# Kernel optimization log

Hardware: AMD Instinct MI355X
Metric: run time of the kernel (lower is better)

## Reference

```python
import jax, jax.numpy as jnp
import numpy as np

IGNORE_INDEX = 255


def setup_inputs() -> dict:
    key = jax.random.key(0)
    k1, k2 = jax.random.split(key)
    n, h, w = 8, 256, 256
    num_class, cnum = 20, 4
    c = num_class * cnum
    P = 8192  # number of parcel segments
    features = jax.random.normal(k1, (n, c, h, w), dtype=jnp.float32)
    parcel = jax.random.randint(k2, (n, h, w), 0, P, dtype=jnp.int32)
    # all pixels of a parcel share one class label (as the torch code assumes)
    target = (parcel % num_class).astype(jnp.int32)
    return {"features": features, "target": target, "parcel": parcel,
            "num_segments": P, "cnum": cnum, "num_class": num_class}


def reference(features, target, parcel, num_segments, cnum, num_class):
    n, c, h, w = features.shape
    hw = h * w
    # n c h w -> n (h w) c
    fea = features.reshape(n, c, hw).transpose(0, 2, 1)
    # MaxPool1d(cnum, stride=cnum) over channel dim: group consecutive cnum channels
    branch_dis = fea.reshape(n, hw, num_class, cnum).max(axis=-1)  # [n, hw, num_class]
    branch_dis = branch_dis.reshape(n * hw, num_class)

    t = target.reshape(-1)
    p = parcel.reshape(-1)
    valid = t != IGNORE_INDEX
    wgt = valid.astype(branch_dis.dtype)

    # fused segment-mean replacing the python loop over unique parcel ids
    seg_sum = jax.ops.segment_sum(branch_dis * wgt[:, None], p, num_segments=num_segments)
    counts = jax.ops.segment_sum(wgt, p, num_segments=num_segments)
    seg_mean = seg_sum / jnp.maximum(counts, 1.0)[:, None]  # [P, num_class]

    # per-parcel target (labels are constant within a parcel -> max == first)
    t_masked = jnp.where(valid, t, -1)
    tgt_parcel = jax.ops.segment_max(t_masked, p, num_segments=num_segments)
    seg_valid = (counts > 0).astype(seg_mean.dtype)

    logp = jax.nn.log_softmax(seg_mean, axis=-1)
    tgt_safe = jnp.clip(tgt_parcel, 0, num_class - 1)
    nll = -jnp.take_along_axis(logp, tgt_safe[:, None], axis=1)[:, 0]
    loss_dis = jnp.sum(nll * seg_valid) / jnp.maximum(jnp.sum(seg_valid), 1.0)

    # diversity branch: softmax over spatial dim, channel-group maxpool
    branch_div = jax.nn.softmax(fea, axis=1)  # softmax over hw
    branch_div = branch_div.reshape(n, hw, num_class, cnum).max(axis=-1)
    loss_div = 1.0 - jnp.mean(jnp.sum(branch_div, axis=1)) / num_class
    return loss_dis, loss_div
```

## Files before the change

### kernel.cpp

```cpp
#include <hip/hip_runtime.h>
#include <float.h>

#define IGNORE_INDEX 255

constexpr int N_IMG = 8;
constexpr int C     = 80;
constexpr int HW    = 65536;
constexpr int NC    = 20;
constexpr int CNUM  = 4;
constexpr int P     = 8192;
constexpr int NPIX  = N_IMG * HW;
constexpr int STRIPES = 4;
constexpr int NCH   = N_IMG * C;

constexpr size_t B_BDS   = 0;
constexpr size_t B_CNT   = (size_t)NPIX * 20 * 4;
constexpr size_t B_ACC   = B_CNT + (size_t)P * 4;
constexpr size_t B_OFF   = B_ACC + 64;
constexpr size_t B_WOFF  = B_OFF + (size_t)P * 4;
constexpr size_t B_PM    = B_WOFF + (size_t)P * 4;
constexpr size_t B_PS    = B_PM + (size_t)NCH * STRIPES * 4;
constexpr size_t B_CHOFF = B_PS + (size_t)NCH * STRIPES * 4;
constexpr size_t B_TGT   = B_CHOFF + (size_t)NCH * 4;
constexpr size_t NEED    = B_TGT + (size_t)P * 4;

__device__ __forceinline__ float waveMax(float v) {
#pragma unroll
  for (int o = 32; o > 0; o >>= 1) v = fmaxf(v, __shfl_down(v, o, 64));
  return v;
}
__device__ __forceinline__ float waveSum(float v) {
#pragma unroll
  for (int o = 32; o > 0; o >>= 1) v += __shfl_down(v, o, 64);
  return v;
}

__global__ __launch_bounds__(256) void stats_hist_kernel(
    const float* __restrict__ f, const int* __restrict__ target,
    const int* __restrict__ parcel, float* __restrict__ pm,
    float* __restrict__ ps, int* __restrict__ cnt) {
  if (blockIdx.x >= NCH * STRIPES) {
    const int t4 = (blockIdx.x - NCH * STRIPES) * 256 + threadIdx.x;
    const int4 tv = ((const int4*)target)[t4];
    const int4 pv = ((const int4*)parcel)[t4];
    if (tv.x != IGNORE_INDEX) atomicAdd(&cnt[pv.x], 1);
    if (tv.y != IGNORE_INDEX) atomicAdd(&cnt[pv.y], 1);
    if (tv.z != IGNORE_INDEX) atomicAdd(&cnt[pv.z], 1);
    if (tv.w != IGNORE_INDEX) atomicAdd(&cnt[pv.w], 1);
    return;
  }
  const int ch = blockIdx.x >> 2, stripe = blockIdx.x & 3;
  const float4* base =
      (const float4*)(f + (size_t)ch * HW + (size_t)stripe * (HW / STRIPES));
  const int n4 = HW / STRIPES / 4;
  float m = -FLT_MAX;
  for (int i = threadIdx.x; i < n4; i += 256) {
    float4 v = base[i];
    m = fmaxf(m, fmaxf(fmaxf(v.x, v.y), fmaxf(v.z, v.w)));
  }
  __shared__ float sred[4];
  __shared__ float bcast;
  const int wid = threadIdx.x >> 6, lid = threadIdx.x & 63;
  float wm = waveMax(m);
  if (lid == 0) sred[wid] = wm;
  __syncthreads();
  if (threadIdx.x == 0)
    bcast = fmaxf(fmaxf(sred[0], sred[1]), fmaxf(sred[2], sred[3]));
  __syncthreads();
  const float M = bcast;
  float s = 0.f;
  for (int i = threadIdx.x; i < n4; i += 256) {
    float4 v = base[i];
    s += __expf(v.x - M) + __expf(v.y - M) + __expf(v.z - M) + __expf(v.w - M);
  }
  float wsv = waveSum(s);
  __syncthreads();
  if (lid == 0) sred[wid] = wsv;
  __syncthreads();
  if (threadIdx.x == 0) {
    pm[blockIdx.x] = M;
    ps[blockIdx.x] = sred[0] + sred[1] + sred[2] + sred[3];
  }
}

__global__ __launch_bounds__(1024) void combine_scan_kernel(
    const float* __restrict__ pm, const float* __restrict__ ps,
    float* __restrict__ choff, const int* __restrict__ cnt,
    int* __restrict__ offs, int* __restrict__ woff) {
  const int t = threadIdx.x;
  if (t < NCH) {
    float m = -FLT_MAX;
#pragma unroll
    for (int i = 0; i < STRIPES; i++) m = fmaxf(m, pm[t * STRIPES + i]);
    float s = 0.f;
#pragma unroll
    for (int i = 0; i < STRIPES; i++)
      s += ps[t * STRIPES + i] * __expf(pm[t * STRIPES + i] - m);
    choff[t] = m + logf(s);
  }
  __shared__ int sh[1024];
  const int4* c4 = (const int4*)(cnt + t * 8);
  int4 a = c4[0], b = c4[1];
  int c[8] = {a.x, a.y, a.z, a.w, b.x, b.y, b.z, b.w};
  int tot = 0;
#pragma unroll
  for (int j = 0; j < 8; j++) tot += c[j];
  sh[t] = tot;
  __syncthreads();
  for (int d = 1; d < 1024; d <<= 1) {
    int v = (t >= d) ? sh[t - d] : 0;
    __syncthreads();
    sh[t] += v;
    __syncthreads();
  }
  int e = sh[t] - tot;
#pragma unroll
  for (int j = 0; j < 8; j++) {
    offs[t * 8 + j] = e;
    woff[t * 8 + j] = e;
    e += c[j];
  }
}

__global__ __launch_bounds__(256) void divbd_scatter_kernel(
    const float* __restrict__ f, const int* __restrict__ target,
    const int* __restrict__ parcel, const float* __restrict__ choff,
    int* __restrict__ woff, float* __restrict__ bds, int* __restrict__ tgtp,
    float* __restrict__ div_acc) {
  const int pg = blockIdx.x * 256 + threadIdx.x;
  const int img = pg >> 16;
  const int pix = pg & (HW - 1);
  const float* fb = f + (size_t)img * C * HW + pix;
  __shared__ float soff[C];
  if (threadIdx.x < C) soff[threadIdx.x] = choff[img * C + threadIdx.x];
  __syncthreads();
  float dm[NC];
  float divs = 0.f;
#pragma unroll
  for (int k = 0; k < NC; k++) {
    float d = -FLT_MAX, e = -FLT_MAX;
#pragma unroll
    for (int j = 0; j < CNUM; j++) {
      const int ch = k * CNUM + j;
      float v = fb[(size_t)ch * HW];
      d = fmaxf(d, v);
      e = fmaxf(e, v - soff[ch]);
    }
    dm[k] = d;
    divs += __expf(e);
  }
  const int t = target[pg];
  const int p = parcel[pg];
  if (t != IGNORE_INDEX) {
    const int pos = atomicAdd(&woff[p], 1);
    float4* o = (float4*)(bds + (size_t)pos * NC);
    o[0] = make_float4(dm[0], dm[1], dm[2], dm[3]);
    o[1] = make_float4(dm[4], dm[5], dm[6], dm[7]);
    o[2] = make_float4(dm[8], dm[9], dm[10], dm[11]);
    o[3] = make_float4(dm[12], dm[13], dm[14], dm[15]);
    o[4] = make_float4(dm[16], dm[17], dm[18], dm[19]);
    tgtp[p] = t;
  }
  __shared__ float sred[4];
  const int wid = threadIdx.x >> 6, lid = threadIdx.x & 63;
  float wsum = waveSum(divs);
  if (lid == 0) sred[wid] = wsum;
  __syncthreads();
  if (threadIdx.x == 0)
    atomicAdd(div_acc, sred[0] + sred[1] + sred[2] + sred[3]);
}

__global__ __launch_bounds__(256) void parcel_kernel(
    const float* __restrict__ bds, const int* __restrict__ cnt,
    const int* __restrict__ offs, const int* __restrict__ tgtp,
    float* __restrict__ acc) {
  const int wid = threadIdx.x >> 6, lid = threadIdx.x & 63;
  const int p = blockIdx.x * 4 + wid;
  const int c = cnt[p];
  float sums[NC];
#pragma unroll
  for (int k = 0; k < NC; k++) sums[k] = 0.f;
  if (c > 0) {
    const int start = offs[p];
    for (int i = lid; i < c; i += 64) {
      const float4* b = (const float4*)(bds + (size_t)(start + i) * NC);
      float4 b0 = b[0], b1 = b[1], b2 = b[2], b3 = b[3], b4 = b[4];
      sums[0] += b0.x;  sums[1] += b0.y;  sums[2] += b0.z;  sums[3] += b0.w;
      sums[4] += b1.x;  sums[5] += b1.y;  sums[6] += b1.z;  sums[7] += b1.w;
      sums[8] += b2.x;  sums[9] += b2.y;  sums[10] += b2.z; sums[11] += b2.w;
      sums[12] += b3.x; sums[13] += b3.y; sums[14] += b3.z; sums[15] += b3.w;
      sums[16] += b4.x; sums[17] += b4.y; sums[18] += b4.z; sums[19] += b4.w;
    }
  }
#pragma unroll
  for (int o = 32; o > 0; o >>= 1) {
#pragma unroll
    for (int k = 0; k < NC; k++) sums[k] += __shfl_xor(sums[k], o, 64);
  }
  float nll = 0.f, val = 0.f;
  if (c > 0) {
    const float inv = 1.f / (float)c;
    float mean[NC];
    float m = -FLT_MAX;
#pragma unroll
    for (int k = 0; k < NC; k++) {
      mean[k] = sums[k] * inv;
      m = fmaxf(m, mean[k]);
    }
    float se = 0.f;
#pragma unroll
    for (int k = 0; k < NC; k++) se += __expf(mean[k] - m);
    const float lse = m + logf(se);
    const int t = min(max(tgtp[p], 0), NC - 1);
    nll = lse - mean[t];
    val = 1.f;
  }
  __shared__ float sn[4], sv[4];
  if (lid == 0) { sn[wid] = nll; sv[wid] = val; }
  __syncthreads();
  if (threadIdx.x == 0) {
    atomicAdd(&acc[1], sn[0] + sn[1] + sn[2] + sn[3]);
    atomicAdd(&acc[2], sv[0] + sv[1] + sv[2] + sv[3]);
  }
}

__global__ void finalize_kernel(const float* __restrict__ acc,
                                float* __restrict__ out) {
  out[0] = acc[1] / fmaxf(acc[2], 1.f);
  out[1] = 1.f - acc[0] / (float)(N_IMG * NC * NC);
}

constexpr size_t OFF_SEGSUM = 0;
constexpr size_t OFF_COUNTS = 163840;
constexpr size_t OFF_CHOFF  = 172032;
constexpr size_t OFF_ACC    = 172672;
constexpr size_t BYTE_TGT   = 690752;
constexpr size_t BYTE_ZERO  = 690752;
constexpr size_t BYTE_TGT_N = P * sizeof(int);

__global__ __launch_bounds__(256) void chan_stats_fb(
    const float* __restrict__ f, float* __restrict__ chan_off) {
  const int ch = blockIdx.x;
  const float4* base = (const float4*)(f + (size_t)ch * HW);
  const int n4 = HW / 4;
  float m = -FLT_MAX;
  for (int i = threadIdx.x; i < n4; i += 256) {
    float4 v = base[i];
    m = fmaxf(m, fmaxf(fmaxf(v.x, v.y), fmaxf(v.z, v.w)));
  }
  __shared__ float sred[4];
  __shared__ float bcast;
  const int wid = threadIdx.x >> 6, lid = threadIdx.x & 63;
  float wm = waveMax(m);
  if (lid == 0) sred[wid] = wm;
  __syncthreads();
  if (threadIdx.x == 0)
    bcast = fmaxf(fmaxf(sred[0], sred[1]), fmaxf(sred[2], sred[3]));
  __syncthreads();
  const float M = bcast;
  float s = 0.f;
  for (int i = threadIdx.x; i < n4; i += 256) {
    float4 v = base[i];
    s += __expf(v.x - M) + __expf(v.y - M) + __expf(v.z - M) + __expf(v.w - M);
  }
  float wsv = waveSum(s);
  __syncthreads();
  if (lid == 0) sred[wid] = wsv;
  __syncthreads();
  if (threadIdx.x == 0)
    chan_off[ch] = M + logf(sred[0] + sred[1] + sred[2] + sred[3]);
}

__global__ __launch_bounds__(256) void pixel_fb(
    const float* __restrict__ f, const int* __restrict__ target,
    const int* __restrict__ parcel, const float* __restrict__ chan_off,
    float* __restrict__ seg_sum, float* __restrict__ counts,
    int* __restrict__ tgtp, float* __restrict__ div_acc) {
  const int t4 = blockIdx.x * 256 + threadIdx.x;
  const int img = t4 / (HW / 4);
  const int pix0 = (t4 % (HW / 4)) * 4;
  const float* fb = f + (size_t)img * C * HW;
  __shared__ float soff[C];
  if (threadIdx.x < C) soff[threadIdx.x] = chan_off[img * C + threadIdx.x];
  __syncthreads();
  const int4 tv = *(const int4*)(target + (size_t)img * HW + pix0);
  const int4 pv = *(const int4*)(parcel + (size_t)img * HW + pix0);
  int tarr[4] = {tv.x, tv.y, tv.z, tv.w};
  int parr[4] = {pv.x, pv.y, pv.z, pv.w};
  bool val[4];
#pragma unroll
  for (int i = 0; i < 4; i++) val[i] = (tarr[i] != IGNORE_INDEX);
  float divs = 0.f;
#pragma unroll
  for (int k = 0; k < NC; k++) {
    float4 dmax = make_float4(-FLT_MAX, -FLT_MAX, -FLT_MAX, -FLT_MAX);
    float4 em = make_float4(-FLT_MAX, -FLT_MAX, -FLT_MAX, -FLT_MAX);
#pragma unroll
    for (int j = 0; j < CNUM; j++) {
      const int ch = k * CNUM + j;
      float4 v = *(const float4*)(fb + (size_t)ch * HW + pix0);
      const float off = soff[ch];
      dmax.x = fmaxf(dmax.x, v.x); dmax.y = fmaxf(dmax.y, v.y);
      dmax.z = fmaxf(dmax.z, v.z); dmax.w = fmaxf(dmax.w, v.w);
      em.x = fmaxf(em.x, v.x - off); em.y = fmaxf(em.y, v.y - off);
      em.z = fmaxf(em.z, v.z - off); em.w = fmaxf(em.w, v.w - off);
    }
    divs += __expf(em.x) + __expf(em.y) + __expf(em.z) + __expf(em.w);
    float dmv[4] = {dmax.x, dmax.y, dmax.z, dmax.w};
#pragma unroll
    for (int i = 0; i < 4; i++)
      if (val[i]) atomicAdd(&seg_sum[parr[i] * NC + k], dmv[i]);
  }
#pragma unroll
  for (int i = 0; i < 4; i++) {
    if (val[i]) {
      atomicAdd(&counts[parr[i]], 1.0f);
      atomicMax(&tgtp[parr[i]], tarr[i]);
    }
  }
  __shared__ float sred[4];
  const int wid = threadIdx.x >> 6, lid = threadIdx.x & 63;
  float wsum = waveSum(divs);
  if (lid == 0) sred[wid] = wsum;
  __syncthreads();
  if (threadIdx.x == 0)
    atomicAdd(div_acc, sred[0] + sred[1] + sred[2] + sred[3]);
}

__global__ __launch_bounds__(256) void seg_fb(
    const float* __restrict__ seg_sum, const float* __restrict__ counts,
    const int* __restrict__ tgtp, float* __restrict__ nll_acc,
    float* __restrict__ vcnt_acc) {
  const int s = blockIdx.x * 256 + threadIdx.x;
  const float cntv = counts[s];
  const float valid = (cntv > 0.f) ? 1.f : 0.f;
  const float inv = 1.f / fmaxf(cntv, 1.f);
  float mean[NC];
  float m = -FLT_MAX;
#pragma unroll
  for (int k = 0; k < NC; k++) {
    mean[k] = seg_sum[s * NC + k] * inv;
    m = fmaxf(m, mean[k]);
  }
  float se = 0.f;
#pragma unroll
  for (int k = 0; k < NC; k++) se += __expf(mean[k] - m);
  const float lse = m + logf(se);
  int t = tgtp[s];
  t = min(max(t, 0), NC - 1);
  const float nll = (lse - mean[t]) * valid;
  __shared__ float sn[4], sv[4];
  const int wid = threadIdx.x >> 6, lid = threadIdx.x & 63;
  float wn = waveSum(nll);
  float wv = waveSum(valid);
  if (lid == 0) { sn[wid] = wn; sv[wid] = wv; }
  __syncthreads();
  if (threadIdx.x == 0) {
    atomicAdd(nll_acc, sn[0] + sn[1] + sn[2] + sn[3]);
    atomicAdd(vcnt_acc, sv[0] + sv[1] + sv[2] + sv[3]);
  }
}

extern "C" void kernel_launch(void* const* d_in, const int* in_sizes, int n_in,
                              void* d_out, int out_size, void* d_ws,
                              size_t ws_size, hipStream_t stream) {
  const float* features = (const float*)d_in[0];
  const int*   target   = (const int*)d_in[1];
  const int*   parcel   = (const int*)d_in[2];
  float* out = (float*)d_out;
  char* wsb = (char*)d_ws;

  if (ws_size >= NEED) {
    float* bds   = (float*)(wsb + B_BDS);
    int*   cnt   = (int*)(wsb + B_CNT);
    float* acc   = (float*)(wsb + B_ACC);
    int*   offs  = (int*)(wsb + B_OFF);
    int*   woff  = (int*)(wsb + B_WOFF);
    float* pm    = (float*)(wsb + B_PM);
    float* ps    = (float*)(wsb + B_PS);
    float* choff = (float*)(wsb + B_CHOFF);
    int*   tgtp  = (int*)(wsb + B_TGT);

    hipMemsetAsync(wsb + B_CNT, 0, P * 4 + 64, stream);

    stats_hist_kernel<<<NCH * STRIPES + NPIX / 1024, 256, 0, stream>>>(
        features, target, parcel, pm, ps, cnt);
    combine_scan_kernel<<<1, 1024, 0, stream>>>(pm, ps, choff, cnt, offs,
                                                woff);
    divbd_scatter_kernel<<<NPIX / 256, 256, 0, stream>>>(
        features, target, parcel, choff, woff, bds, tgtp, acc + 0);
    parcel_kernel<<<P / 4, 256, 0, stream>>>(bds, cnt, offs, tgtp, acc);
    finalize_kernel<<<1, 1, 0, stream>>>(acc, out);
  } else {
    float* ws       = (float*)d_ws;
    float* seg_sum  = ws + OFF_SEGSUM;
    float* counts   = ws + OFF_COUNTS;
    float* chan_off = ws + OFF_CHOFF;
    float* acc      = ws + OFF_ACC;
    int*   tgtp     = (int*)(wsb + BYTE_TGT);

    hipMemsetAsync(d_ws, 0, BYTE_ZERO, stream);
    hipMemsetAsync(wsb + BYTE_TGT, 0xFF, BYTE_TGT_N, stream);
    chan_stats_fb<<<NCH, 256, 0, stream>>>(features, chan_off);
    pixel_fb<<<NPIX / 4 / 256, 256, 0, stream>>>(features, target, parcel,
                                                 chan_off, seg_sum, counts,
                                                 tgtp, acc + 0);
    seg_fb<<<P / 256, 256, 0, stream>>>(seg_sum, counts, tgtp, acc + 1,
                                        acc + 2);
    finalize_kernel<<<1, 1, 0, stream>>>(acc, out);
  }
}
```

Before: 381.6 us.

## Write maxpool results densely by pixel and scatter only indices per parcel

```diff
diff --git a/kernel.cpp b/kernel.cpp
--- a/kernel.cpp
+++ b/kernel.cpp
@@ -13,8 +13,9 @@
 constexpr int STRIPES = 4;
 constexpr int NCH   = N_IMG * C;
 
-constexpr size_t B_BDS   = 0;
-constexpr size_t B_CNT   = (size_t)NPIX * 20 * 4;
+constexpr size_t B_DM    = 0;
+constexpr size_t B_SIDX  = (size_t)NPIX * 20 * 4;
+constexpr size_t B_CNT   = B_SIDX + (size_t)NPIX * 4;
 constexpr size_t B_ACC   = B_CNT + (size_t)P * 4;
 constexpr size_t B_OFF   = B_ACC + 64;
 constexpr size_t B_WOFF  = B_OFF + (size_t)P * 4;
@@ -52,12 +53,13 @@
   const int ch = blockIdx.x >> 2, stripe = blockIdx.x & 3;
   const float4* base =
       (const float4*)(f + (size_t)ch * HW + (size_t)stripe * (HW / STRIPES));
-  const int n4 = HW / STRIPES / 4;
+  float4 r[16];
+#pragma unroll
+  for (int i = 0; i < 16; i++) r[i] = base[threadIdx.x + (i << 8)];
   float m = -FLT_MAX;
-  for (int i = threadIdx.x; i < n4; i += 256) {
-    float4 v = base[i];
-    m = fmaxf(m, fmaxf(fmaxf(v.x, v.y), fmaxf(v.z, v.w)));
-  }
+#pragma unroll
+  for (int i = 0; i < 16; i++)
+    m = fmaxf(m, fmaxf(fmaxf(r[i].x, r[i].y), fmaxf(r[i].z, r[i].w)));
   __shared__ float sred[4];
   __shared__ float bcast;
   const int wid = threadIdx.x >> 6, lid = threadIdx.x & 63;
@@ -69,10 +71,10 @@
   __syncthreads();
   const float M = bcast;
   float s = 0.f;
-  for (int i = threadIdx.x; i < n4; i += 256) {
-    float4 v = base[i];
-    s += __expf(v.x - M) + __expf(v.y - M) + __expf(v.z - M) + __expf(v.w - M);
-  }
+#pragma unroll
+  for (int i = 0; i < 16; i++)
+    s += __expf(r[i].x - M) + __expf(r[i].y - M) + __expf(r[i].z - M) +
+         __expf(r[i].w - M);
   float wsv = waveSum(s);
   __syncthreads();
   if (lid == 0) sred[wid] = wsv;
@@ -122,44 +124,61 @@
   }
 }
 
+__device__ __forceinline__ float4 max4(float4 a, float4 b) {
+  return make_float4(fmaxf(a.x, b.x), fmaxf(a.y, b.y), fmaxf(a.z, b.z),
+                     fmaxf(a.w, b.w));
+}
+
 __global__ __launch_bounds__(256) void divbd_scatter_kernel(
     const float* __restrict__ f, const int* __restrict__ target,
     const int* __restrict__ parcel, const float* __restrict__ choff,
-    int* __restrict__ woff, float* __restrict__ bds, int* __restrict__ tgtp,
-    float* __restrict__ div_acc) {
-  const int pg = blockIdx.x * 256 + threadIdx.x;
-  const int img = pg >> 16;
-  const int pix = pg & (HW - 1);
-  const float* fb = f + (size_t)img * C * HW + pix;
+    int* __restrict__ woff, float* __restrict__ dmall, int* __restrict__ sidx,
+    int* __restrict__ tgtp, float* __restrict__ div_acc) {
+  const int tid = blockIdx.x * 256 + threadIdx.x;
+  const int img = tid >> 14;
+  const int pix0 = (tid & 16383) << 2;
+  const float* fb = f + (size_t)img * C * HW + pix0;
   __shared__ float soff[C];
   if (threadIdx.x < C) soff[threadIdx.x] = choff[img * C + threadIdx.x];
   __syncthreads();
-  float dm[NC];
+  const int pgbase = (img << 16) + pix0;
   float divs = 0.f;
 #pragma unroll
-  for (int k = 0; k < NC; k++) {
-    float d = -FLT_MAX, e = -FLT_MAX;
-#pragma unroll
-    for (int j = 0; j < CNUM; j++) {
-      const int ch = k * CNUM + j;
-      float v = fb[(size_t)ch * HW];
-      d = fmaxf(d, v);
-      e = fmaxf(e, v - soff[ch]);
-    }
-    dm[k] = d;
-    divs += __expf(e);
-  }
-  const int t = target[pg];
-  const int p = parcel[pg];
-  if (t != IGNORE_INDEX) {
-    const int pos = atomicAdd(&woff[p], 1);
-    float4* o = (float4*)(bds + (size_t)pos * NC);
-    o[0] = make_float4(dm[0], dm[1], dm[2], dm[3]);
-    o[1] = make_float4(dm[4], dm[5], dm[6], dm[7]);
-    o[2] = make_float4(dm[8], dm[9], dm[10], dm[11]);
-    o[3] = make_float4(dm[12], dm[13], dm[14], dm[15]);
-    o[4] = make_float4(dm[16], dm[17], dm[18], dm[19]);
-    tgtp[p] = t;
+  for (int kc = 0; kc < 5; kc++) {
+    float4 dmg[4];
+#pragma unroll
+    for (int g = 0; g < 4; g++) {
+      const int k = kc * 4 + g;
+      float4 d = make_float4(-FLT_MAX, -FLT_MAX, -FLT_MAX, -FLT_MAX);
+      float4 e = make_float4(-FLT_MAX, -FLT_MAX, -FLT_MAX, -FLT_MAX);
+#pragma unroll
+      for (int j = 0; j < CNUM; j++) {
+        const int ch = k * CNUM + j;
+        float4 v = *(const float4*)(fb + (size_t)ch * HW);
+        const float off = soff[ch];
+        d = max4(d, v);
+        e = max4(e, make_float4(v.x - off, v.y - off, v.z - off, v.w - off));
+      }
+      dmg[g] = d;
+      divs += __expf(e.x) + __expf(e.y) + __expf(e.z) + __expf(e.w);
+    }
+    float4* ob = (float4*)dmall + (size_t)pgbase * 5 + kc;
+    ob[0]  = make_float4(dmg[0].x, dmg[1].x, dmg[2].x, dmg[3].x);
+    ob[5]  = make_float4(dmg[0].y, dmg[1].y, dmg[2].y, dmg[3].y);
+    ob[10] = make_float4(dmg[0].z, dmg[1].z, dmg[2].z, dmg[3].z);
+    ob[15] = make_float4(dmg[0].w, dmg[1].w, dmg[2].w, dmg[3].w);
+  }
+  const int4 tv = *(const int4*)(target + pgbase);
+  const int4 pv = *(const int4*)(parcel + pgbase);
+  const int ts[4] = {tv.x, tv.y, tv.z, tv.w};
+  const int pa[4] = {pv.x, pv.y, pv.z, pv.w};
+#pragma unroll
+  for (int r = 0; r < 4; r++) {
+    if (ts[r] != IGNORE_INDEX) {
+      const int pos = atomicAdd(&woff[pa[r]], 1);
+      sidx[pos] = pgbase + r;
+      tgtp[pa[r]] = ts[r];
+    }
   }
   __shared__ float sred[4];
   const int wid = threadIdx.x >> 6, lid = threadIdx.x & 63;
@@ -171,9 +190,9 @@
 }
 
 __global__ __launch_bounds__(256) void parcel_kernel(
-    const float* __restrict__ bds, const int* __restrict__ cnt,
-    const int* __restrict__ offs, const int* __restrict__ tgtp,
-    float* __restrict__ acc) {
+    const float* __restrict__ dmall, const int* __restrict__ cnt,
+    const int* __restrict__ offs, const int* __restrict__ sidx,
+    const int* __restrict__ tgtp, float* __restrict__ acc) {
   const int wid = threadIdx.x >> 6, lid = threadIdx.x & 63;
   const int p = blockIdx.x * 4 + wid;
   const int c = cnt[p];
@@ -183,7 +202,8 @@
   if (c > 0) {
     const int start = offs[p];
     for (int i = lid; i < c; i += 64) {
-      const float4* b = (const float4*)(bds + (size_t)(start + i) * NC);
+      const int pg = sidx[start + i];
+      const float4* b = (const float4*)dmall + (size_t)pg * 5;
       float4 b0 = b[0], b1 = b[1], b2 = b[2], b3 = b[3], b4 = b[4];
       sums[0] += b0.x;  sums[1] += b0.y;  sums[2] += b0.z;  sums[3] += b0.w;
       sums[4] += b1.x;  sums[5] += b1.y;  sums[6] += b1.z;  sums[7] += b1.w;
@@ -371,7 +391,8 @@
   char* wsb = (char*)d_ws;
 
   if (ws_size >= NEED) {
-    float* bds   = (float*)(wsb + B_BDS);
+    float* dmall = (float*)(wsb + B_DM);
+    int*   sidx  = (int*)(wsb + B_SIDX);
     int*   cnt   = (int*)(wsb + B_CNT);
     float* acc   = (float*)(wsb + B_ACC);
     int*   offs  = (int*)(wsb + B_OFF);
@@ -387,9 +408,10 @@
         features, target, parcel, pm, ps, cnt);
     combine_scan_kernel<<<1, 1024, 0, stream>>>(pm, ps, choff, cnt, offs,
                                                 woff);
-    divbd_scatter_kernel<<<NPIX / 256, 256, 0, stream>>>(
-        features, target, parcel, choff, woff, bds, tgtp, acc + 0);
-    parcel_kernel<<<P / 4, 256, 0, stream>>>(bds, cnt, offs, tgtp, acc);
+    divbd_scatter_kernel<<<NPIX / 4 / 256, 256, 0, stream>>>(
+        features, target, parcel, choff, woff, dmall, sidx, tgtp, acc + 0);
+    parcel_kernel<<<P / 4, 256, 0, stream>>>(dmall, cnt, offs, sidx, tgtp,
+                                             acc);
     finalize_kernel<<<1, 1, 0, stream>>>(acc, out);
   } else {
     float* ws       = (float*)d_ws;
```

After: 389.0 us. No clear change (+1.9%).
